# Optimization experiments

Hardware: AMD Instinct MI355X
Metric: run time of the kernel (lower is better)

Reference implementation:

```python
import jax, jax.numpy as jnp
import numpy as np

B, S, D, H = 2, 2048, 1024, 16
HD = D // H


def setup_inputs() -> dict:
    key = jax.random.key(0)
    ks = jax.random.split(key, 5)
    scale = 0.02
    x = jax.random.normal(ks[0], (B, S, D), dtype=jnp.float32)
    Wq = jax.random.normal(ks[1], (D, D), dtype=jnp.float32) * scale
    Wk = jax.random.normal(ks[2], (D, D), dtype=jnp.float32) * scale
    Wv = jax.random.normal(ks[3], (D, D), dtype=jnp.float32) * scale
    Wo = jax.random.normal(ks[4], (D, D), dtype=jnp.float32) * scale
    z = jnp.zeros((D,), dtype=jnp.float32)
    return {"x": x, "Wq": Wq, "bq": z, "Wk": Wk, "bk": z, "Wv": Wv, "bv": z, "Wo": Wo, "bo": z}


def reference(x, Wq, bq, Wk, bk, Wv, bv, Wo, bo):
    b, s, d = x.shape
    hd = d // H
    # QKV projections -> [b, H, s, hd]
    def heads(W, bias):
        return (x @ W.T + bias).reshape(b, s, H, hd).transpose(0, 2, 1, 3)
    q = heads(Wq, bq)
    k = heads(Wk, bk)
    v = heads(Wv, bv)
    scale = 1.0 / np.sqrt(hd).astype(np.float32)
    attn = scale * jnp.einsum('bhqd,bhkd->bhqk', q, k)  # [b,H,s,s]
    # causal mask (attn dropout p=0 is identity before masking)
    causal = jnp.tril(jnp.ones((s, s), dtype=bool))
    attn = jnp.where(causal[None, None], attn, -jnp.inf)
    attn = jax.nn.softmax(attn, axis=-1)
    ans = jnp.einsum('bhqk,bhkd->bhqd', attn, v)
    ans = ans.transpose(0, 2, 1, 3).reshape(b, s, d)
    return ans @ Wo.T + bo
```

## Files before the change

kernel.cpp:

```cpp
#include <hip/hip_runtime.h>

#define DEV __device__ __forceinline__

typedef __attribute__((ext_vector_type(8))) __bf16 bf16x8;
typedef __attribute__((ext_vector_type(4))) float f32x4;
typedef __attribute__((ext_vector_type(16))) float f32x16;
typedef __attribute__((ext_vector_type(4))) unsigned short u16x4;
typedef __attribute__((ext_vector_type(8))) unsigned short u16x8;
typedef __attribute__((ext_vector_type(2))) unsigned u32x2;

DEV unsigned short f2bf(float f) {
  unsigned u = __builtin_bit_cast(unsigned, f);
  u += 0x7FFFu + ((u >> 16) & 1u);
  return (unsigned short)(u >> 16);
}

DEV f32x4 mfma16(bf16x8 a, bf16x8 b, f32x4 c) {
  return __builtin_amdgcn_mfma_f32_16x16x32_bf16(a, b, c, 0, 0, 0);
}
DEV f32x16 mfma32(bf16x8 a, bf16x8 b, f32x16 c) {
  return __builtin_amdgcn_mfma_f32_32x32x16_bf16(a, b, c, 0, 0, 0);
}

DEV void gload16(const void* g, void* l) {
  __builtin_amdgcn_global_load_lds(
      (const __attribute__((address_space(1))) unsigned int*)g,
      (__attribute__((address_space(3))) unsigned int*)l, 16, 0, 0);
}

DEV void plswap(unsigned& x, unsigned& y) {
#if __has_builtin(__builtin_amdgcn_permlane32_swap)
  u32x2 r = __builtin_amdgcn_permlane32_swap(x, y, false, false);
  x = r[0];
  y = r[1];
#else
  unsigned sx = __shfl_xor(x, 32, 64), sy = __shfl_xor(y, 32, 64);
  int hi = (threadIdx.x & 63) >> 5;
  unsigned nx = hi ? sy : x;
  unsigned ny = hi ? y : sx;
  x = nx;
  y = ny;
#endif
}
DEV float xadd32(float v) {
  unsigned a = __builtin_bit_cast(unsigned, v), b = a;
  plswap(a, b);
  return __builtin_bit_cast(float, a) + __builtin_bit_cast(float, b);
}

__global__ __launch_bounds__(256) void k_cvt_all(
    const float* __restrict__ x,
    const float* __restrict__ Wq, const float* __restrict__ Wk,
    const float* __restrict__ Wv, const float* __restrict__ Wo,
    unsigned short* __restrict__ xb,
    unsigned short* __restrict__ Wqb, unsigned short* __restrict__ Wkb,
    unsigned short* __restrict__ Wvb, unsigned short* __restrict__ Wob) {
  int g = blockIdx.x * 256 + threadIdx.x;
  const float* src;
  unsigned short* dst;
  int loc;
  if (g < 524288) {
    src = x; dst = xb; loc = g;
  } else {
    int r = g - 524288;
    int w = r >> 17;
    loc = r & 131071;
    src = w == 0 ? Wq : w == 1 ? Wk : w == 2 ? Wv : Wo;
    dst = w == 0 ? Wqb : w == 1 ? Wkb : w == 2 ? Wvb : Wob;
  }
  int row = loc >> 7, k8 = loc & 127;
  const f32x4* s = (const f32x4*)(src + ((size_t)row << 10) + (k8 << 3));
  f32x4 a = s[0], b = s[1];
  u16x8 o;
  o[0] = f2bf(a[0]); o[1] = f2bf(a[1]); o[2] = f2bf(a[2]); o[3] = f2bf(a[3]);
  o[4] = f2bf(b[0]); o[5] = f2bf(b[1]); o[6] = f2bf(b[2]); o[7] = f2bf(b[3]);
  *(u16x8*)(dst + ((size_t)row << 10) + ((k8 << 3) ^ ((row & 7) << 3))) = o;
}

DEV void gemm_mainloop(const char* Ag, const char* Bg, char* lds,
                       int lane, int wid, f32x4 acc[4][4]) {
  int g4 = lane >> 4, r16 = lane & 15;
  int wm = wid >> 1, wn = wid & 1;
  int adA[2], adB[2];
#pragma unroll
  for (int ks = 0; ks < 2; ++ks) {
    int swz = ((ks * 4 + g4) ^ (lane & 7)) << 4;
    adA[ks] = (wm * 64 + r16) * 128 + swz;
    adB[ks] = 16384 + (wn * 64 + r16) * 128 + swz;
  }
  int o0 = wid * 4096 + lane * 16;
  int grow[4], ginr[4];
#pragma unroll
  for (int i = 0; i < 4; ++i) {
    grow[i] = (o0 + i * 1024) >> 7;
    ginr[i] = (o0 + i * 1024) & 127;
  }
  auto STAGE = [&](int KT, int BASE) {
#pragma unroll
    for (int i = 0; i < 4; ++i) {
      int oo = o0 + i * 1024;
      size_t gofs = (size_t)grow[i] * 2048 + (size_t)KT * 128 + ginr[i];
      gload16(Ag + gofs, lds + BASE + oo);
      gload16(Bg + gofs, lds + BASE + 16384 + oo);
    }
  };
  STAGE(0, 0);
  __syncthreads();
  for (int kt = 0; kt < 16; ++kt) {
    int cur = (kt & 1) << 15;
    if (kt + 1 < 16) STAGE(kt + 1, cur ^ 32768);
#pragma unroll
    for (int ks = 0; ks < 2; ++ks) {
      bf16x8 af[4], bfr[4];
#pragma unroll
      for (int i = 0; i < 4; ++i) {
        af[i]  = *(const bf16x8*)(lds + cur + adA[ks] + i * 2048);
        bfr[i] = *(const bf16x8*)(lds + cur + adB[ks] + i * 2048);
      }
#pragma unroll
      for (int mi = 0; mi < 4; ++mi)
#pragma unroll
        for (int ni = 0; ni < 4; ++ni)
          acc[mi][ni] = mfma16(af[mi], bfr[ni], acc[mi][ni]);
    }
    __syncthreads();
  }
}

__global__ __launch_bounds__(256) void k_gemm_qkv(
    const unsigned short* __restrict__ xb,
    const unsigned short* __restrict__ Wqb, const unsigned short* __restrict__ Wkb,
    const unsigned short* __restrict__ Wvb,
    const float* __restrict__ bq, const float* __restrict__ bk,
    const float* __restrict__ bv,
    unsigned short* __restrict__ Qb, unsigned short* __restrict__ Kb,
    unsigned short* __restrict__ Vt) {
  __shared__ char lds[65536];
  int tid = threadIdx.x, lane = tid & 63, wid = tid >> 6;
  int bm = blockIdx.x & 31, bn = blockIdx.x >> 5;
  int r0 = bm * 128;
  int colT = bn * 128;
  int which = colT >> 10;
  int ncol = colT & 1023;
  const unsigned short* Wb = which == 0 ? Wqb : which == 1 ? Wkb : Wvb;
  f32x4 acc[4][4] = {};
  gemm_mainloop((const char*)xb + (size_t)r0 * 2048,
                (const char*)Wb + (size_t)ncol * 2048, lds, lane, wid, acc);
  int g4 = lane >> 4, r16 = lane & 15, wm = wid >> 1, wn = wid & 1;
  const float* bias = which == 0 ? bq : which == 1 ? bk : bv;
  float oscale = which == 0 ? 0.18033688f : 1.0f;
  int ncolw = ncol + wn * 64;
#pragma unroll
  for (int ni = 0; ni < 4; ++ni) {
    int gcol = ncolw + ni * 16 + r16;
    float bvv = bias[gcol];
    int h = gcol >> 6, hd = gcol & 63;
#pragma unroll
    for (int mi = 0; mi < 4; ++mi) {
      int growb = r0 + wm * 64 + mi * 16 + g4 * 4;
      int bb = growb >> 11, s0 = growb & 2047;
      if (which == 2) {
        u16x4 pk;
#pragma unroll
        for (int jj = 0; jj < 4; ++jj) pk[jj] = f2bf(acc[mi][ni][jj] + bvv);
        *(u16x4*)(Vt + ((size_t)(bb * 16 + h) * 64 + hd) * 2048 + s0) = pk;
      } else {
        unsigned short* dst = which == 0 ? Qb : Kb;
        size_t base = ((size_t)(bb * 16 + h) * 2048 + s0) * 64 + hd;
#pragma unroll
        for (int jj = 0; jj < 4; ++jj)
          dst[base + (size_t)jj * 64] = f2bf((acc[mi][ni][jj] + bvv) * oscale);
      }
    }
  }
}

__global__ __launch_bounds__(128) void k_attn(
    const unsigned short* __restrict__ Q, const unsigned short* __restrict__ K,
    const unsigned short* __restrict__ Vt, unsigned short* __restrict__ ansb) {
  __shared__ char lds[2 * 16384 + 256];
  int tid = threadIdx.x, lane = tid & 63, wid = tid >> 6;
  int l31 = lane & 31, hi = lane >> 5;
  int bid = blockIdx.x;
  int bh = (bid & 7) * 4 + ((bid >> 3) & 3);
  int g = bid >> 5;
  int chunk = g < 8 ? g : g < 16 ? 39 - g : g < 24 ? 31 - g : g - 8;
  int b = bh >> 4, h = bh & 15;
  int q0 = chunk * 64 + wid * 32;
  int nt = chunk + 1;
  const unsigned short* Qh = Q + (size_t)bh * (2048 * 64);
  const char* Kg = (const char*)(K + (size_t)bh * (2048 * 64));
  const char* Vg = (const char*)(Vt + (size_t)bh * (64 * 2048));
  char* wb = lds + 32768 + wid * 128;

  int kof[4], ko[4], vo[4];
#pragma unroll
  for (int i = 0; i < 4; ++i) {
    int o = tid * 16 + i * 2048;
    int row = o >> 7, c = o & 127;
    int sc = c ^ ((row & 7) << 4);
    kof[i] = o;
    ko[i] = row * 128 + sc;
    vo[i] = row * 4096 + sc;
  }

  bf16x8 qf[4];
#pragma unroll
  for (int ks = 0; ks < 4; ++ks)
    qf[ks] = *(const bf16x8*)(Qh + (size_t)(q0 + l31) * 64 + ks * 16 + hi * 8);

  f32x16 O0 = {}, O1 = {}, l16 = {};
  int swzl = (l31 & 7) << 4;
  int hioff = hi * 16;

  auto STAGEA = [&](int T, int BASE) {
    size_t kK = (size_t)T * 8192;
    size_t kV = (size_t)T * 128;
#pragma unroll
    for (int i = 0; i < 4; ++i) {
      gload16(Kg + kK + ko[i], lds + BASE + kof[i]);
      gload16(Vg + kV + vo[i], lds + BASE + 8192 + kof[i]);
    }
  };

  STAGEA(0, 0);
  __syncthreads();
  for (int t = 0; t < nt; ++t) {
    int cur = (t & 1) << 14;
    if (t + 1 < nt) STAGEA(t + 1, cur ^ 16384);
    const char* KL = lds + cur;
    const char* VL = KL + 8192;
    int kv0 = t * 64;
    f32x16 s0 = {}, s1 = {};
    __builtin_amdgcn_s_setprio(1);
#pragma unroll
    for (int ks = 0; ks < 4; ++ks) {
      bf16x8 kf0 = *(const bf16x8*)(KL + l31 * 128 + ((ks * 32 + hioff) ^ swzl));
      bf16x8 kf1 = *(const bf16x8*)(KL + (32 + l31) * 128 + ((ks * 32 + hioff) ^ swzl));
      s0 = mfma32(kf0, qf[ks], s0);
      s1 = mfma32(kf1, qf[ks], s1);
    }
    __builtin_amdgcn_s_setprio(0);
    if (kv0 + 63 > q0) {
      int lim2 = q0 + l31 - kv0 - 4 * hi;
#pragma unroll
      for (int r = 0; r < 16; ++r) {
        int kc = (r & 3) + 8 * (r >> 2);
        if (kc > lim2) s0[r] = -1e30f;
        if (kc + 32 > lim2) s1[r] = -1e30f;
      }
    }
#pragma unroll
    for (int r = 0; r < 16; ++r) {
      s0[r] = __builtin_amdgcn_exp2f(s0[r]);
      s1[r] = __builtin_amdgcn_exp2f(s1[r]);
      l16[r] += s0[r] + s1[r];
    }
    __builtin_amdgcn_s_setprio(1);
#define PV_CHUNK(SV, E, C16) { \
    unsigned x0, x1, y0, y1; \
    asm("v_cvt_pk_bf16_f32 %0, %1, %2" : "=v"(x0) : "v"(SV[8*(E)+0]), "v"(SV[8*(E)+1])); \
    asm("v_cvt_pk_bf16_f32 %0, %1, %2" : "=v"(x1) : "v"(SV[8*(E)+2]), "v"(SV[8*(E)+3])); \
    asm("v_cvt_pk_bf16_f32 %0, %1, %2" : "=v"(y0) : "v"(SV[8*(E)+4]), "v"(SV[8*(E)+5])); \
    asm("v_cvt_pk_bf16_f32 %0, %1, %2" : "=v"(y1) : "v"(SV[8*(E)+6]), "v"(SV[8*(E)+7])); \
    plswap(x0, y0); \
    plswap(x1, y1); \
    union { unsigned u[4]; bf16x8 v; } pf; \
    pf.u[0] = x0; \
    pf.u[1] = x1; \
    pf.u[2] = y0; \
    pf.u[3] = y1; \
    bf16x8 v0 = *(const bf16x8*)(VL + l31 * 128 + (((C16) * 32 + hioff) ^ swzl)); \
    bf16x8 v1 = *(const bf16x8*)(VL + (32 + l31) * 128 + (((C16) * 32 + hioff) ^ swzl)); \
    O0 = mfma32(pf.v, v0, O0); \
    O1 = mfma32(pf.v, v1, O1); }
    PV_CHUNK(s0, 0, 0)
    PV_CHUNK(s0, 1, 1)
    PV_CHUNK(s1, 0, 2)
    PV_CHUNK(s1, 1, 3)
#undef PV_CHUNK
    __builtin_amdgcn_s_setprio(0);
    __syncthreads();
  }
  float a[16];
#pragma unroll
  for (int r = 0; r < 16; ++r) a[r] = l16[r];
#pragma unroll
  for (int st2 = 8; st2 >= 1; st2 >>= 1)
#pragma unroll
    for (int i = 0; i < st2; ++i) a[i] += a[i + st2];
  float lf = xadd32(a[0]);
  float rl = 1.f / lf;
  if (lane < 32) *(float*)(wb + l31 * 4) = rl;
  asm volatile("s_waitcnt lgkmcnt(0)" ::: "memory");
  f32x4 rv0 = *(const f32x4*)(wb + hioff);
  f32x4 rv1 = *(const f32x4*)(wb + 32 + hioff);
  f32x4 rv2 = *(const f32x4*)(wb + 64 + hioff);
  f32x4 rv3 = *(const f32x4*)(wb + 96 + hioff);
#pragma unroll
  for (int r = 0; r < 16; ++r) {
    float sc = (r < 4 ? rv0 : r < 8 ? rv1 : r < 12 ? rv2 : rv3)[r & 3];
    int rowl = q0 + (r & 3) + 8 * (r >> 2) + 4 * hi;
    int rowg = (b << 11) + rowl;
    int cswz = (rowl & 7) << 3;
    int cg0 = (h << 6) + l31;
    int cg1 = (h << 6) + 32 + l31;
    ansb[(size_t)rowg * 1024 + (cg0 ^ cswz)] = f2bf(O0[r] * sc);
    ansb[(size_t)rowg * 1024 + (cg1 ^ cswz)] = f2bf(O1[r] * sc);
  }
}

__global__ __launch_bounds__(256) void k_gemm_out(
    const unsigned short* __restrict__ ansb, const unsigned short* __restrict__ Wob,
    const float* __restrict__ bo, float* __restrict__ out) {
  __shared__ char lds[65536];
  int tid = threadIdx.x, lane = tid & 63, wid = tid >> 6;
  int bm = blockIdx.x & 31, bn = blockIdx.x >> 5;
  int r0 = bm * 128, c0 = bn * 128;
  f32x4 acc[4][4] = {};
  gemm_mainloop((const char*)ansb + (size_t)r0 * 2048,
                (const char*)Wob + (size_t)c0 * 2048, lds, lane, wid, acc);
  int g4 = lane >> 4, r16 = lane & 15, wm = wid >> 1, wn = wid & 1;
#pragma unroll
  for (int ni = 0; ni < 4; ++ni) {
    int gcol = c0 + wn * 64 + ni * 16 + r16;
    float bvv = bo[gcol];
#pragma unroll
    for (int mi = 0; mi < 4; ++mi) {
      int growb = r0 + wm * 64 + mi * 16 + g4 * 4;
#pragma unroll
      for (int jj = 0; jj < 4; ++jj)
        out[(size_t)(growb + jj) * 1024 + gcol] = acc[mi][ni][jj] + bvv;
    }
  }
}

extern "C" void kernel_launch(void* const* d_in, const int* in_sizes, int n_in,
                              void* d_out, int out_size, void* d_ws, size_t ws_size,
                              hipStream_t stream) {
  const float* x  = (const float*)d_in[0];
  const float* Wq = (const float*)d_in[1];
  const float* bq = (const float*)d_in[2];
  const float* Wk = (const float*)d_in[3];
  const float* bk = (const float*)d_in[4];
  const float* Wv = (const float*)d_in[5];
  const float* bv = (const float*)d_in[6];
  const float* Wo = (const float*)d_in[7];
  const float* bo = (const float*)d_in[8];
  char* ws = (char*)d_ws;
  unsigned short* xb   = (unsigned short*)(ws);
  unsigned short* ansb = (unsigned short*)(ws);
  unsigned short* Wqb  = (unsigned short*)(ws + (8u  << 20));
  unsigned short* Wkb  = (unsigned short*)(ws + (10u << 20));
  unsigned short* Wvb  = (unsigned short*)(ws + (12u << 20));
  unsigned short* Wob  = (unsigned short*)(ws + (14u << 20));
  unsigned short* Qb   = (unsigned short*)(ws + (16u << 20));
  unsigned short* Kb   = (unsigned short*)(ws + (24u << 20));
  unsigned short* Vt   = (unsigned short*)(ws + (32u << 20));

  k_cvt_all<<<4096, 256, 0, stream>>>(x, Wq, Wk, Wv, Wo, xb, Wqb, Wkb, Wvb, Wob);
  k_gemm_qkv<<<768, 256, 0, stream>>>(xb, Wqb, Wkb, Wvb, bq, bk, bv, Qb, Kb, Vt);
  k_attn<<<1024, 128, 0, stream>>>(Qb, Kb, Vt, ansb);
  k_gemm_out<<<256, 256, 0, stream>>>(ansb, Wob, bo, (float*)d_out);
}
```

Measured before the change: 108.4 us.

## Split long causal attention chunks into two KV segments with a combine kernel

Query chunks 16-31 have their KV range split into two halves, each handled by its own block, which writes unnormalized fp32 partial outputs and row sums to workspace. A new combine kernel adds the partials, normalizes, and writes bf16 output. Short chunks are still computed directly. This shortens the longest blocks and evens out work across the 1536-block grid, at the cost of an extra kernel launch and fp32 partial traffic. No running max is kept, so combining partials by plain summation is consistent with the existing unmasked exp2 softmax.

```diff
diff --git a/kernel.cpp b/kernel.cpp
--- a/kernel.cpp
+++ b/kernel.cpp
@@ -177,17 +177,23 @@
 
 __global__ __launch_bounds__(128) void k_attn(
     const unsigned short* __restrict__ Q, const unsigned short* __restrict__ K,
-    const unsigned short* __restrict__ Vt, unsigned short* __restrict__ ansb) {
+    const unsigned short* __restrict__ Vt, unsigned short* __restrict__ ansb,
+    float* __restrict__ PO, float* __restrict__ PL) {
   __shared__ char lds[2 * 16384 + 256];
   int tid = threadIdx.x, lane = tid & 63, wid = tid >> 6;
   int l31 = lane & 31, hi = lane >> 5;
   int bid = blockIdx.x;
   int bh = (bid & 7) * 4 + ((bid >> 3) & 3);
-  int g = bid >> 5;
-  int chunk = g < 8 ? g : g < 16 ? 39 - g : g < 24 ? 31 - g : g - 8;
+  int s = bid >> 5;
+  int c, t0, t1;
+  bool direct;
+  if (s < 16)      { c = 16 + s; t0 = 0;            t1 = (c + 2) >> 1; direct = false; }
+  else if (s < 32) { c = s;      t0 = (c + 2) >> 1; t1 = c + 1;        direct = false; }
+  else             { c = 47 - s; t0 = 0;            t1 = c + 1;        direct = true;  }
+  int seg = (s < 32 && s >= 16) ? 1 : 0;
+  int pidx = (bh * 16 + (c - 16)) * 2 + seg;
   int b = bh >> 4, h = bh & 15;
-  int q0 = chunk * 64 + wid * 32;
-  int nt = chunk + 1;
+  int q0 = c * 64 + wid * 32;
   const unsigned short* Qh = Q + (size_t)bh * (2048 * 64);
   const char* Kg = (const char*)(K + (size_t)bh * (2048 * 64));
   const char* Vg = (const char*)(Vt + (size_t)bh * (64 * 2048));
@@ -197,8 +203,8 @@
 #pragma unroll
   for (int i = 0; i < 4; ++i) {
     int o = tid * 16 + i * 2048;
-    int row = o >> 7, c = o & 127;
-    int sc = c ^ ((row & 7) << 4);
+    int row = o >> 7, cc = o & 127;
+    int sc = cc ^ ((row & 7) << 4);
     kof[i] = o;
     ko[i] = row * 128 + sc;
     vo[i] = row * 4096 + sc;
@@ -223,14 +229,13 @@
     }
   };
 
-  STAGEA(0, 0);
+  STAGEA(t0, 0);
   __syncthreads();
-  for (int t = 0; t < nt; ++t) {
-    int cur = (t & 1) << 14;
-    if (t + 1 < nt) STAGEA(t + 1, cur ^ 16384);
+  for (int t = t0; t < t1; ++t) {
+    int cur = ((t - t0) & 1) << 14;
+    if (t + 1 < t1) STAGEA(t + 1, cur ^ 16384);
     const char* KL = lds + cur;
     const char* VL = KL + 8192;
-    int kv0 = t * 64;
     f32x16 s0 = {}, s1 = {};
     __builtin_amdgcn_s_setprio(1);
 #pragma unroll
@@ -241,8 +246,8 @@
       s1 = mfma32(kf1, qf[ks], s1);
     }
     __builtin_amdgcn_s_setprio(0);
-    if (kv0 + 63 > q0) {
-      int lim2 = q0 + l31 - kv0 - 4 * hi;
+    if (t == c) {
+      int lim2 = q0 + l31 - t * 64 - 4 * hi;
 #pragma unroll
       for (int r = 0; r < 16; ++r) {
         int kc = (r & 3) + 8 * (r >> 2);
@@ -290,24 +295,68 @@
 #pragma unroll
     for (int i = 0; i < st2; ++i) a[i] += a[i + st2];
   float lf = xadd32(a[0]);
-  float rl = 1.f / lf;
-  if (lane < 32) *(float*)(wb + l31 * 4) = rl;
-  asm volatile("s_waitcnt lgkmcnt(0)" ::: "memory");
-  f32x4 rv0 = *(const f32x4*)(wb + hioff);
-  f32x4 rv1 = *(const f32x4*)(wb + 32 + hioff);
-  f32x4 rv2 = *(const f32x4*)(wb + 64 + hioff);
-  f32x4 rv3 = *(const f32x4*)(wb + 96 + hioff);
-#pragma unroll
-  for (int r = 0; r < 16; ++r) {
-    float sc = (r < 4 ? rv0 : r < 8 ? rv1 : r < 12 ? rv2 : rv3)[r & 3];
-    int rowl = q0 + (r & 3) + 8 * (r >> 2) + 4 * hi;
-    int rowg = (b << 11) + rowl;
-    int cswz = (rowl & 7) << 3;
-    int cg0 = (h << 6) + l31;
-    int cg1 = (h << 6) + 32 + l31;
-    ansb[(size_t)rowg * 1024 + (cg0 ^ cswz)] = f2bf(O0[r] * sc);
-    ansb[(size_t)rowg * 1024 + (cg1 ^ cswz)] = f2bf(O1[r] * sc);
-  }
+  if (direct) {
+    float rl = 1.f / lf;
+    if (lane < 32) *(float*)(wb + l31 * 4) = rl;
+    asm volatile("s_waitcnt lgkmcnt(0)" ::: "memory");
+    f32x4 rv0 = *(const f32x4*)(wb + hioff);
+    f32x4 rv1 = *(const f32x4*)(wb + 32 + hioff);
+    f32x4 rv2 = *(const f32x4*)(wb + 64 + hioff);
+    f32x4 rv3 = *(const f32x4*)(wb + 96 + hioff);
+#pragma unroll
+    for (int r = 0; r < 16; ++r) {
+      float sc = (r < 4 ? rv0 : r < 8 ? rv1 : r < 12 ? rv2 : rv3)[r & 3];
+      int rowl = q0 + (r & 3) + 8 * (r >> 2) + 4 * hi;
+      int rowg = (b << 11) + rowl;
+      int cswz = (rowl & 7) << 3;
+      int cg0 = (h << 6) + l31;
+      int cg1 = (h << 6) + 32 + l31;
+      ansb[(size_t)rowg * 1024 + (cg0 ^ cswz)] = f2bf(O0[r] * sc);
+      ansb[(size_t)rowg * 1024 + (cg1 ^ cswz)] = f2bf(O1[r] * sc);
+    }
+  } else {
+    float* po = PO + (size_t)pidx * 4096;
+#pragma unroll
+    for (int r = 0; r < 16; ++r) {
+      int rowl = wid * 32 + (r & 3) + 8 * (r >> 2) + 4 * hi;
+      po[rowl * 64 + l31] = O0[r];
+      po[rowl * 64 + 32 + l31] = O1[r];
+    }
+    if (hi == 0) PL[pidx * 64 + wid * 32 + l31] = lf;
+  }
+}
+
+__global__ __launch_bounds__(256) void k_attn_combine(
+    const float* __restrict__ PO, const float* __restrict__ PL,
+    unsigned short* __restrict__ ansb) {
+  int bid = blockIdx.x;
+  int bh = bid & 31, cc = 16 + (bid >> 5);
+  int b = bh >> 4, h = bh & 15;
+  int t = threadIdx.x;
+  int r = t >> 2, c4 = (t & 3) << 4;
+  int pbase = (bh * 16 + (cc - 16)) * 2;
+  const float* A = PO + (size_t)pbase * 4096 + r * 64 + c4;
+  const float* B = A + 4096;
+  float la = PL[pbase * 64 + r];
+  float lb = PL[(pbase + 1) * 64 + r];
+  float rl = 1.f / (la + lb);
+  f32x4 s0 = *(const f32x4*)(A + 0) + *(const f32x4*)(B + 0);
+  f32x4 s1 = *(const f32x4*)(A + 4) + *(const f32x4*)(B + 4);
+  f32x4 s2 = *(const f32x4*)(A + 8) + *(const f32x4*)(B + 8);
+  f32x4 s3 = *(const f32x4*)(A + 12) + *(const f32x4*)(B + 12);
+  u16x8 o0, o1;
+#pragma unroll
+  for (int j = 0; j < 4; ++j) {
+    o0[j] = f2bf(s0[j] * rl);
+    o0[4 + j] = f2bf(s1[j] * rl);
+    o1[j] = f2bf(s2[j] * rl);
+    o1[4 + j] = f2bf(s3[j] * rl);
+  }
+  int rowg = (b << 11) + cc * 64 + r;
+  int colg = (h << 6) + c4;
+  int cswz = (rowg & 7) << 3;
+  *(u16x8*)(ansb + (size_t)rowg * 1024 + (colg ^ cswz)) = o0;
+  *(u16x8*)(ansb + (size_t)rowg * 1024 + ((colg + 8) ^ cswz)) = o1;
 }
 
 __global__ __launch_bounds__(256) void k_gemm_out(
@@ -357,9 +406,12 @@
   unsigned short* Qb   = (unsigned short*)(ws + (16u << 20));
   unsigned short* Kb   = (unsigned short*)(ws + (24u << 20));
   unsigned short* Vt   = (unsigned short*)(ws + (32u << 20));
+  float*          PO   = (float*)(ws + (40u << 20));
+  float*          PL   = (float*)(ws + (56u << 20));
 
   k_cvt_all<<<4096, 256, 0, stream>>>(x, Wq, Wk, Wv, Wo, xb, Wqb, Wkb, Wvb, Wob);
   k_gemm_qkv<<<768, 256, 0, stream>>>(xb, Wqb, Wkb, Wvb, bq, bk, bv, Qb, Kb, Vt);
-  k_attn<<<1024, 128, 0, stream>>>(Qb, Kb, Vt, ansb);
+  k_attn<<<1536, 128, 0, stream>>>(Qb, Kb, Vt, ansb, PO, PL);
+  k_attn_combine<<<512, 256, 0, stream>>>(PO, PL, ansb);
   k_gemm_out<<<256, 256, 0, stream>>>(ansb, Wob, bo, (float*)d_out);
 }
```

New measurement: 107.5 us. About the same (-0.8%).
